# Kernel tuning notes

Hardware: AMD Instinct MI355X
Metric: run time of the kernel (lower is better)

The kernel has to match this reference:

```python
import jax, jax.numpy as jnp
import numpy as np

# HNMS hyperparameters (from init_kwargs)
W0, H0 = 16.0, 16.0
ALPHA = 0.7
GAMMA = 0.6
BX, BY = 0.5, 0.5   # b_is_relative=True -> offsets in cell units
N = 2_000_000

CODE_OFF = 4096      # offset so quantized codes are non-negative
CODE_RANGE = 8192    # 13 bits per code -> two codes fit in one int32 key


def _hash_keys(rects):
    """Hash each (cx, cy, w, h) box to a bucket id, packed as two int32 keys.

    Scale hashing: iw = round(log(w/w0)/log(alpha)) (same for h).
    Spatial hashing: cell size = gamma * w0 * alpha**iw; relative offset bx.
    """
    cx, cy, w, h = rects[:, 0], rects[:, 1], rects[:, 2], rects[:, 3]
    inv_log_alpha = 1.0 / jnp.log(jnp.float32(ALPHA))
    iw = jnp.round(jnp.log(w / W0) * inv_log_alpha).astype(jnp.int32)
    ih = jnp.round(jnp.log(h / H0) * inv_log_alpha).astype(jnp.int32)
    cell_w = GAMMA * W0 * jnp.power(jnp.float32(ALPHA), iw.astype(jnp.float32))
    cell_h = GAMMA * H0 * jnp.power(jnp.float32(ALPHA), ih.astype(jnp.float32))
    ix = jnp.round(cx / cell_w - BX).astype(jnp.int32)
    iy = jnp.round(cy / cell_h - BY).astype(jnp.int32)

    def pack(a, b):
        a = jnp.clip(a + CODE_OFF, 0, CODE_RANGE - 1)
        b = jnp.clip(b + CODE_OFF, 0, CODE_RANGE - 1)
        return a * CODE_RANGE + b  # fits easily in int32

    key_hi = pack(ix, iy)   # spatial bucket
    key_lo = pack(iw, ih)   # scale bucket
    return key_hi, key_lo


def _hnms(rects, conf):
    key_hi, key_lo = _hash_keys(rects)
    n = conf.shape[0]
    # Sort by bucket (hi, lo), then by descending conf, index for determinism.
    order = jnp.lexsort((jnp.arange(n), -conf, key_lo, key_hi))
    sh = key_hi[order]
    sl = key_lo[order]
    first = jnp.concatenate(
        [jnp.ones((1,), bool), (sh[1:] != sh[:-1]) | (sl[1:] != sl[:-1])]
    )
    keep = jnp.zeros((n,), bool).at[order].set(first)
    kept_conf = conf * keep  # suppressed boxes get score 0
    return kept_conf, keep


def setup_inputs() -> dict:
    key = jax.random.key(0)
    k1, k2, k3 = jax.random.split(key, 3)
    cxcy = jax.random.uniform(k1, (N, 2), jnp.float32, 0.0, 1333.0)
    wh = jax.random.uniform(k2, (N, 2), jnp.float32, 4.0, 256.0)
    rects = jnp.concatenate([cxcy, wh], axis=1)  # [N,4] (cx, cy, w, h)
    conf = jax.random.uniform(k3, (N,), jnp.float32, 0.01, 1.0)
    return {"rects": rects, "conf": conf}


def reference(rects, conf):
    kept_conf, keep = _hnms(rects, conf)
    return kept_conf, keep
```

## Files before the change

### kernel.cpp

```cpp
#include <hip/hip_runtime.h>
#include <stdint.h>


struct HashParams { int nx[13]; int cum[13]; float cell[13]; int T; };

#define TBL_BITS 22
#define TBL_SLOTS (1u << TBL_BITS)
#define TBL_MASK  (TBL_SLOTS - 1u)
#define SWZ_MUL   0x9E3779B1u

__device__ __forceinline__ unsigned long long pack_val(float conf, unsigned int i) {
    return ((unsigned long long)__float_as_uint(conf) << 32)
         | (unsigned long long)(~i);
}

__global__ __launch_bounds__(256)
void hnms_insert(const float4* __restrict__ rects,
                 const float*  __restrict__ conf,
                 unsigned long long* __restrict__ tvals,
                 unsigned int* __restrict__ slot_of,
                 int n, HashParams P)
{
    __shared__ int   s_nx[13], s_cum[13];
    __shared__ float s_cell[13];
    int t = threadIdx.x;
    if (t < 13) { s_nx[t] = P.nx[t]; s_cum[t] = P.cum[t]; s_cell[t] = P.cell[t]; }
    __syncthreads();

    int i = blockIdx.x * blockDim.x + t;
    if (i >= n) return;

    float4 r = rects[i];

    const float log_alpha = (float)log((double)0.7f);
    const float inv_log_a = 1.0f / log_alpha;
    float lw = (float)log((double)(r.z * 0.0625f));
    float lh = (float)log((double)(r.w * 0.0625f));
    int iw = (int)rintf(lw * inv_log_a);
    int ih = (int)rintf(lh * inv_log_a);

    int kw = min(max(iw + 8, 0), 12);
    int kh = min(max(ih + 8, 0), 12);
    float cell_w = s_cell[kw];
    float cell_h = s_cell[kh];
    int ix = (int)rintf(r.x / cell_w - 0.5f);
    int iy = (int)rintf(r.y / cell_h - 0.5f);

    int nxw = s_nx[kw];
    ix = min(max(ix, 0), nxw - 1);
    iy = min(max(iy, 0), s_nx[kh] - 1);

    unsigned int raw  = (unsigned int)(s_cum[kw] * P.T + nxw * s_cum[kh]
                                       + iy * nxw + ix);
    unsigned int slot = (raw * SWZ_MUL) & TBL_MASK;

    unsigned long long mine = pack_val(conf[i], (unsigned int)i);
    unsigned long long cur  = __hip_atomic_load(&tvals[slot], __ATOMIC_RELAXED,
                                                __HIP_MEMORY_SCOPE_AGENT);
    if (cur < mine)
        atomicMax(&tvals[slot], mine);
    slot_of[i] = slot;
}

__global__ __launch_bounds__(256)
void hnms_resolve(const float* __restrict__ conf,
                  const unsigned long long* __restrict__ tvals,
                  const unsigned int* __restrict__ slot_of,
                  float* __restrict__ out_conf,
                  float* __restrict__ out_keep,
                  int n)
{
    int i = blockIdx.x * blockDim.x + threadIdx.x;
    if (i >= n) return;

    float c = conf[i];
    bool keep = (tvals[slot_of[i]] == pack_val(c, (unsigned int)i));
    out_conf[i] = keep ? c : 0.0f;
    out_keep[i] = keep ? 1.0f : 0.0f;
}

extern "C" void kernel_launch(void* const* d_in, const int* in_sizes, int n_in,
                              void* d_out, int out_size, void* d_ws, size_t ws_size,
                              hipStream_t stream)
{
    const float* rects = (const float*)d_in[0];
    const float* conf  = (const float*)d_in[1];
    const int n = in_sizes[1];

    HashParams P;
    {
        int off = 0;
        for (int k = 0; k < 13; ++k) {
            int iw = k - 8;
            float p32  = (float)pow((double)0.7f, (double)iw);
            float cell = 9.6f * p32;
            int nxk = (int)rint(1333.0 / (double)cell - 0.5) + 1 + 3;
            P.cell[k] = cell;
            P.nx[k]   = nxk;
            P.cum[k]  = off;
            off += nxk;
        }
        P.T = off;
    }

    unsigned long long* tvals = (unsigned long long*)d_ws;
    unsigned int*       slots = (unsigned int*)(tvals + TBL_SLOTS);

    hipMemsetAsync(tvals, 0x00, (size_t)TBL_SLOTS * 8, stream);

    float* out_conf = (float*)d_out;
    float* out_keep = out_conf + n;

    const int block = 256;
    const int grid  = (n + block - 1) / block;
    hnms_insert<<<grid, block, 0, stream>>>(
        (const float4*)rects, conf, tvals, slots, n, P);
    hnms_resolve<<<grid, block, 0, stream>>>(
        conf, tvals, slots, out_conf, out_keep, n);
}
```

Measured before the change: 140.3 us.

## Replace per-box resolve with table sweep scattering winners into zeroed outputs

Result: no change. 140.0 us (-0.2%).

```diff
diff --git a/kernel.cpp b/kernel.cpp
--- a/kernel.cpp
+++ b/kernel.cpp
@@ -18,7 +18,6 @@
 void hnms_insert(const float4* __restrict__ rects,
                  const float*  __restrict__ conf,
                  unsigned long long* __restrict__ tvals,
-                 unsigned int* __restrict__ slot_of,
                  int n, HashParams P)
 {
     __shared__ int   s_nx[13], s_cum[13];
@@ -59,24 +58,28 @@
                                                 __HIP_MEMORY_SCOPE_AGENT);
     if (cur < mine)
         atomicMax(&tvals[slot], mine);
-    slot_of[i] = slot;
 }
 
 __global__ __launch_bounds__(256)
-void hnms_resolve(const float* __restrict__ conf,
-                  const unsigned long long* __restrict__ tvals,
-                  const unsigned int* __restrict__ slot_of,
-                  float* __restrict__ out_conf,
-                  float* __restrict__ out_keep,
-                  int n)
+void hnms_sweep(const ulonglong2* __restrict__ tvals2,
+                float* __restrict__ out_conf,
+                float* __restrict__ out_keep)
 {
-    int i = blockIdx.x * blockDim.x + threadIdx.x;
-    if (i >= n) return;
-
-    float c = conf[i];
-    bool keep = (tvals[slot_of[i]] == pack_val(c, (unsigned int)i));
-    out_conf[i] = keep ? c : 0.0f;
-    out_keep[i] = keep ? 1.0f : 0.0f;
+    const unsigned total = TBL_SLOTS / 2;
+    unsigned stride = gridDim.x * blockDim.x;
+    for (unsigned s = blockIdx.x * blockDim.x + threadIdx.x; s < total; s += stride) {
+        ulonglong2 v = tvals2[s];
+        if (v.x) {
+            unsigned idx = ~(unsigned)v.x;
+            out_conf[idx] = __uint_as_float((unsigned)(v.x >> 32));
+            out_keep[idx] = 1.0f;
+        }
+        if (v.y) {
+            unsigned idx = ~(unsigned)v.y;
+            out_conf[idx] = __uint_as_float((unsigned)(v.y >> 32));
+            out_keep[idx] = 1.0f;
+        }
+    }
 }
 
 extern "C" void kernel_launch(void* const* d_in, const int* in_sizes, int n_in,
@@ -104,17 +107,17 @@
     }
 
     unsigned long long* tvals = (unsigned long long*)d_ws;
-    unsigned int*       slots = (unsigned int*)(tvals + TBL_SLOTS);
-
-    hipMemsetAsync(tvals, 0x00, (size_t)TBL_SLOTS * 8, stream);
 
     float* out_conf = (float*)d_out;
     float* out_keep = out_conf + n;
 
+    hipMemsetAsync(tvals, 0x00, (size_t)TBL_SLOTS * 8, stream);
+    hipMemsetAsync(d_out, 0x00, (size_t)2 * n * sizeof(float), stream);
+
     const int block = 256;
     const int grid  = (n + block - 1) / block;
     hnms_insert<<<grid, block, 0, stream>>>(
-        (const float4*)rects, conf, tvals, slots, n, P);
-    hnms_resolve<<<grid, block, 0, stream>>>(
-        conf, tvals, slots, out_conf, out_keep, n);
+        (const float4*)rects, conf, tvals, n, P);
+    hnms_sweep<<<2048, block, 0, stream>>>(
+        (const ulonglong2*)tvals, out_conf, out_keep);
 }
```
